# Performance work log

Measured on AMD Instinct MI355X. Metric: run time of the kernel, lower is better.

The kernel has to match this reference:

```python
import jax, jax.numpy as jnp
import numpy as np


def setup_inputs() -> dict:
    key = jax.random.key(0)
    ks = jax.random.split(key, 5)
    B, C_in, C_out, H, W, k = 16, 64, 64, 256, 256, 16
    scale = 1.0 / (C_in * C_out)
    return {
        "u": jax.random.normal(ks[0], (B, C_in, H, W), dtype=jnp.float32),
        "W_pos_re": scale * jax.random.normal(ks[1], (C_in, C_out, k, k), dtype=jnp.float32),
        "W_pos_im": scale * jax.random.normal(ks[2], (C_in, C_out, k, k), dtype=jnp.float32),
        "W_neg_re": scale * jax.random.normal(ks[3], (C_in, C_out, k, k), dtype=jnp.float32),
        "W_neg_im": scale * jax.random.normal(ks[4], (C_in, C_out, k, k), dtype=jnp.float32),
    }


def reference(u, W_pos_re, W_pos_im, W_neg_re, W_neg_im):
    B, C_in, H, W = u.shape
    C_out = W_pos_re.shape[1]
    k = W_pos_re.shape[2]
    W_half = W // 2 + 1
    k_h = min(k, H // 2)
    k_w = min(k, W_half)

    R_pos = (W_pos_re + 1j * W_pos_im)[:, :, :k_h, :k_w]  # (C_in, C_out, k_h, k_w)
    R_neg = (W_neg_re + 1j * W_neg_im)[:, :, :k_h, :k_w]

    u_hat = jnp.fft.rfft2(u, norm="ortho")  # (B, C_in, H, W_half) complex

    # spectral multiply on retained modes only
    top = jnp.einsum("bchw,cohw->bohw", u_hat[:, :, :k_h, :k_w], R_pos)
    bot = jnp.einsum("bchw,cohw->bohw", u_hat[:, :, H - k_h:, :k_w], R_neg)

    v_hat = jnp.zeros((B, C_out, H, W_half), dtype=u_hat.dtype)
    v_hat = v_hat.at[:, :, :k_h, :k_w].set(top)
    v_hat = v_hat.at[:, :, H - k_h:, :k_w].set(bot)

    return jnp.fft.irfft2(v_hat, s=(H, W), norm="ortho")  # (B, C_out, H, W) real
```

## Files before the change

### kernel.cpp

```cpp
#include <hip/hip_runtime.h>


#define B_    16
#define H_    256
#define W_    256

#define OFF_CT 0
#define OFF_ST 256
#define OFF_RP 512
#define RP_SZ  (4096*512*2)
#define OFF_U  (OFF_RP + RP_SZ)
#define U_SZ   (512*1024*2)
#define OFF_V  (OFF_U + U_SZ)

typedef const __attribute__((address_space(1))) void g_void;
typedef __attribute__((address_space(3))) void l_void;

__device__ __forceinline__ void load_lds16(const float* g, float* l) {
    __builtin_amdgcn_global_load_lds((g_void*)g, (l_void*)l, 16, 0, 0);
}

__global__ void k_twiddle(float* __restrict__ ws) {
    int t = threadIdx.x;
    double a = 2.0 * 3.14159265358979323846 * (double)t / 256.0;
    ws[OFF_CT + t] = (float)cos(a);
    ws[OFF_ST + t] = (float)sin(a);
}

__global__ __launch_bounds__(256) void k_repack(const float* __restrict__ wpr,
                                                const float* __restrict__ wpi,
                                                const float* __restrict__ wnr,
                                                const float* __restrict__ wni,
                                                float* __restrict__ ws) {
    int co = blockIdx.x, t = threadIdx.x;
    int wm = t & 15;
    float norm = (wm == 0 ? 1.f : 2.f) * (1.f / 65536.f);
    size_t src = (size_t)co * 256 + t;
    float2* rp = (float2*)(ws + OFF_RP) + (size_t)co * 512;
    rp[t]       = make_float2(wpr[src] * norm, wpi[src] * norm);
    rp[t + 256] = make_float2(wnr[src] * norm, wni[src] * norm);
}

__global__ __launch_bounds__(256) void k_fwd(const float* __restrict__ u,
                                             const float* __restrict__ ws,
                                             float* __restrict__ U) {
    __shared__ __align__(16) float ut[32][256];
    __shared__ __align__(16) float Pl[32][36];
    __shared__ float ct[256], st[256];
    int t = threadIdx.x, bc = blockIdx.x;
    ct[t] = ws[OFF_CT + t];
    st[t] = ws[OFF_ST + t];
    const float* ub = u + (size_t)bc * 65536;
    int lane = t & 63, w = t >> 6;

    #pragma unroll
    for (int k = 0; k < 8; ++k) {
        int row = w * 8 + k;
        load_lds16(ub + row * 256 + lane * 4, &ut[row][0]);
    }
    __syncthreads();

    int yl = t & 31, h = t >> 5;
    int wm0 = 2 * h, wm1 = wm0 + 1;
    int j0 = 2 * yl;
    float r0r = ct[wm0], r0i = -st[wm0];
    float r1r = ct[wm1], r1i = -st[wm1];
    float t0r0 = ct[(wm0 * j0) & 255], t0i0 = -st[(wm0 * j0) & 255];
    float t1r0 = ct[(wm1 * j0) & 255], t1i0 = -st[(wm1 * j0) & 255];
    float bs  = (h & 1) ? -1.f : 1.f;
    float dsg = (h & 1) ? 1.f : -1.f;

    int wm = t & 15, m1 = t >> 4;
    float q1r = ct[m1], q1i = -st[m1];
    int m2i = (16 - m1) & 255;
    float q2r = ct[m2i], q2i = st[m2i];
    float w1r = 1.f, w1i = 0.f, w2r = 1.f, w2i = 0.f;
    float U1r = 0.f, U1i = 0.f, U2r = 0.f, U2i = 0.f;

    for (int ch = 0; ch < 8; ++ch) {
        asm volatile("s_waitcnt vmcnt(0)" ::: "memory");
        __syncthreads();

        float t0r = t0r0, t0i = t0i0, t1r = t1r0, t1i = t1i0;
        float p0r = 0.f, p0i = 0.f, p1r = 0.f, p1i = 0.f;
        const float* row = &ut[yl][0];
        #pragma unroll 8
        for (int s = 0; s < 64; ++s) {
            int j = j0 + s;
            float u0 = row[j], u1 = row[j + 64], u2 = row[j + 128];
            float u3 = row[(j + 192) & 255];
            float a = u0 + u2, b = u1 + u3, c = u0 - u2, d = u1 - u3;
            float g0 = fmaf(bs, b, a);
            float g1r = c, g1i = dsg * d;
            p0r = fmaf(g0, t0r, p0r);
            p0i = fmaf(g0, t0i, p0i);
            p1r = fmaf(g1r, t1r, fmaf(-g1i, t1i, p1r));
            p1i = fmaf(g1r, t1i, fmaf( g1i, t1r, p1i));
            float n0r = t0r * r0r - t0i * r0i, n0i = t0r * r0i + t0i * r0r;
            float n1r = t1r * r1r - t1i * r1i, n1i = t1r * r1i + t1i * r1r;
            t0r = n0r; t0i = n0i; t1r = n1r; t1i = n1i;
        }
        *(float4*)&Pl[yl][4 * h] = make_float4(p0r, p0i, p1r, p1i);
        __syncthreads();

        if (ch < 7) {
            const float* ub2 = ub + (ch + 1) * 8192;
            #pragma unroll
            for (int k = 0; k < 8; ++k) {
                int rw = w * 8 + k;
                load_lds16(ub2 + rw * 256 + lane * 4, &ut[rw][0]);
            }
        }

        #pragma unroll 4
        for (int yy = 0; yy < 32; ++yy) {
            float2 g = *(float2*)&Pl[yy][2 * wm];
            U1r = fmaf(g.x, w1r, fmaf(-g.y, w1i, U1r));
            U1i = fmaf(g.x, w1i, fmaf( g.y, w1r, U1i));
            U2r = fmaf(g.x, w2r, fmaf(-g.y, w2i, U2r));
            U2i = fmaf(g.x, w2i, fmaf( g.y, w2r, U2i));
            float n1r = w1r * q1r - w1i * q1i, n1i = w1r * q1i + w1i * q1r;
            float n2r = w2r * q2r - w2i * q2i, n2i = w2r * q2i + w2i * q2r;
            w1r = n1r; w1i = n1i; w2r = n2r; w2i = n2i;
        }
    }

    float2* Ug = (float2*)U;
    Ug[(size_t)(m1 * 16 + wm) * 1024 + bc]        = make_float2(U1r, U1i);
    Ug[(size_t)((m1 + 16) * 16 + wm) * 1024 + bc] = make_float2(U2r, U2i);
}

__global__ __launch_bounds__(256) void k_cgemm(float* __restrict__ ws) {
    __shared__ float2 Ul[1024];
    int mw = blockIdx.x, t = threadIdx.x;
    const float2* Ug = (const float2*)(ws + OFF_U) + (size_t)mw * 1024;
    #pragma unroll
    for (int k = 0; k < 4; ++k) Ul[t + 256 * k] = Ug[t + 256 * k];
    __syncthreads();
    int o = t & 63, bq = t >> 6;
    const float2* rp = (const float2*)(ws + OFF_RP);
    float ar[4] = {0.f, 0.f, 0.f, 0.f}, ai[4] = {0.f, 0.f, 0.f, 0.f};
    #pragma unroll 4
    for (int c = 0; c < 64; ++c) {
        float2 R = rp[(size_t)(c * 64 + o) * 512 + mw];
        #pragma unroll
        for (int j = 0; j < 4; ++j) {
            float2 Uv = Ul[(bq * 4 + j) * 64 + c];
            ar[j] = fmaf(Uv.x, R.x, fmaf(-Uv.y, R.y, ar[j]));
            ai[j] = fmaf(Uv.x, R.y, fmaf( Uv.y, R.x, ai[j]));
        }
    }
    float2* Vg = (float2*)(ws + OFF_V);
    #pragma unroll
    for (int j = 0; j < 4; ++j)
        Vg[(size_t)((bq * 4 + j) * 64 + o) * 512 + mw] = make_float2(ar[j], ai[j]);
}

__global__ __launch_bounds__(256) void k_inv(const float* __restrict__ ws,
                                             float* __restrict__ out) {
    __shared__ float Vl[16][68];
    __shared__ float Tl[4][16][36];
    __shared__ float ct[256], st[256];
    int t = threadIdx.x;
    int bo = blockIdx.x >> 2, q = blockIdx.x & 3;
    ct[t] = ws[OFF_CT + t];
    st[t] = ws[OFF_ST + t];
    {
        const float2* Vg = (const float2*)(ws + OFF_V) + (size_t)bo * 512;
        float2 v0 = Vg[t];
        float2 v1 = Vg[t + 256];
        int m = t >> 4, wmv = t & 15;
        Vl[wmv][2 * m]        = v0.x;  Vl[wmv][2 * m + 1]        = v0.y;
        Vl[wmv][2 * (m + 16)] = v1.x;  Vl[wmv][2 * (m + 16) + 1] = v1.y;
    }
    __syncthreads();

    int wm4 = t & 15, yb = t >> 4;
    int y0 = q * 16 + yb;
    float vr[32], vi[32];
    #pragma unroll
    for (int m = 0; m < 32; ++m) { vr[m] = Vl[wm4][2 * m]; vi[m] = Vl[wm4][2 * m + 1]; }
    float cy = ct[y0], sy = st[y0];
    float T0r=0,T0i=0,T1r=0,T1i=0,T2r=0,T2i=0,T3r=0,T3i=0;
    float tr = 1.f, ti = 0.f;
    #pragma unroll
    for (int m = 0; m < 32; ++m) {
        if (m == 16) {
            int i16 = (4096 - 16 * y0) & 255;
            tr = ct[i16]; ti = st[i16];
        }
        float hr = vr[m] * tr - vi[m] * ti;
        float hi = vr[m] * ti + vi[m] * tr;
        const int md = m & 3;
        T0r += hr; T0i += hi;
        if (md == 0)      { T1r += hr; T1i += hi; T2r += hr; T2i += hi; T3r += hr; T3i += hi; }
        else if (md == 1) { T1r -= hi; T1i += hr; T2r -= hr; T2i -= hi; T3r += hi; T3i -= hr; }
        else if (md == 2) { T1r -= hr; T1i -= hi; T2r += hr; T2i += hi; T3r -= hr; T3i -= hi; }
        else              { T1r += hi; T1i -= hr; T2r -= hr; T2i -= hi; T3r -= hi; T3i += hr; }
        float nr = tr * cy - ti * sy, ni = tr * sy + ti * cy;
        tr = nr; ti = ni;
    }
    Tl[0][yb][wm4] = T0r; Tl[0][yb][16 + wm4] = T0i;
    Tl[1][yb][wm4] = T1r; Tl[1][yb][16 + wm4] = T1i;
    Tl[2][yb][wm4] = T2r; Tl[2][yb][16 + wm4] = T2i;
    Tl[3][yb][wm4] = T3r; Tl[3][yb][16 + wm4] = T3i;
    __syncthreads();

    int l = t & 63, wv = t >> 6;
    float c0[16], s0[16];
    #pragma unroll
    for (int wm = 0; wm < 16; ++wm) {
        int idx = (wm * l) & 255;
        c0[wm] = ct[idx]; s0[wm] = st[idx];
    }
    float* ob = out + (size_t)bo * 65536;
    for (int yi = 0; yi < 16; ++yi) {
        int y = wv * 64 + q * 16 + yi;
        float TR[16], TI[16];
        const float4* rowv = (const float4*)&Tl[wv][yi][0];
        #pragma unroll
        for (int qq = 0; qq < 4; ++qq) {
            float4 a = rowv[qq];
            TR[4*qq]=a.x; TR[4*qq+1]=a.y; TR[4*qq+2]=a.z; TR[4*qq+3]=a.w;
            float4 b = rowv[qq + 4];
            TI[4*qq]=b.x; TI[4*qq+1]=b.y; TI[4*qq+2]=b.z; TI[4*qq+3]=b.w;
        }
        #pragma unroll
        for (int k = 0; k < 4; ++k) {
            float a = 0.f;
            #pragma unroll
            for (int wm = 0; wm < 16; ++wm) {
                int p = (k * wm) & 3;
                if (p == 0)      a +=  TR[wm] * c0[wm] - TI[wm] * s0[wm];
                else if (p == 1) a += -TR[wm] * s0[wm] - TI[wm] * c0[wm];
                else if (p == 2) a += -TR[wm] * c0[wm] + TI[wm] * s0[wm];
                else             a +=  TR[wm] * s0[wm] + TI[wm] * c0[wm];
            }
            ob[(size_t)y * 256 + 64 * k + l] = a;
        }
    }
}

extern "C" void kernel_launch(void* const* d_in, const int* in_sizes, int n_in,
                              void* d_out, int out_size, void* d_ws, size_t ws_size,
                              hipStream_t stream) {
    const float* u   = (const float*)d_in[0];
    const float* wpr = (const float*)d_in[1];
    const float* wpi = (const float*)d_in[2];
    const float* wnr = (const float*)d_in[3];
    const float* wni = (const float*)d_in[4];
    float* out = (float*)d_out;
    float* ws  = (float*)d_ws;

    hipLaunchKernelGGL(k_twiddle, dim3(1),    dim3(256), 0, stream, ws);
    hipLaunchKernelGGL(k_repack,  dim3(4096), dim3(256), 0, stream, wpr, wpi, wnr, wni, ws);
    hipLaunchKernelGGL(k_fwd,     dim3(1024), dim3(256), 0, stream, u, ws, ws + OFF_U);
    hipLaunchKernelGGL(k_cgemm,   dim3(512),  dim3(256), 0, stream, ws);
    hipLaunchKernelGGL(k_inv,     dim3(4096), dim3(256), 0, stream, ws, out);
}
```

Measured before the change: 254.7 us.

## Double-buffer k_fwd input rows and remap row DFT with DPP lane reductions

The forward transform kernel now keeps two LDS buffers for input row chunks and prefetches chunk ch+2 while chunk ch is computed. Each lane now loads 8 contiguous columns once, evaluates all 16 retained width modes in registers, and sums partial results across 8 lanes with DPP shuffles. This replaces the old strided per-mode LDS reads and full-block barriers. In exchange it uses more registers (launch_bounds 2), doubles the LDS input buffer, and relies on manual vmcnt/lgkmcnt waits for correctness.

```diff
diff --git a/kernel.cpp b/kernel.cpp
--- a/kernel.cpp
+++ b/kernel.cpp
@@ -18,6 +18,12 @@
 
 __device__ __forceinline__ void load_lds16(const float* g, float* l) {
     __builtin_amdgcn_global_load_lds((g_void*)g, (l_void*)l, 16, 0, 0);
+}
+
+template<int CTRL>
+__device__ __forceinline__ float dppf(float x) {
+    return __int_as_float(__builtin_amdgcn_update_dpp(
+        0, __float_as_int(x), CTRL, 0xF, 0xF, true));
 }
 
 __global__ void k_twiddle(float* __restrict__ ws) {
@@ -41,10 +47,10 @@
     rp[t + 256] = make_float2(wnr[src] * norm, wni[src] * norm);
 }
 
-__global__ __launch_bounds__(256) void k_fwd(const float* __restrict__ u,
-                                             const float* __restrict__ ws,
-                                             float* __restrict__ U) {
-    __shared__ __align__(16) float ut[32][256];
+__global__ __launch_bounds__(256, 2) void k_fwd(const float* __restrict__ u,
+                                                const float* __restrict__ ws,
+                                                float* __restrict__ U) {
+    __shared__ __align__(16) float ut[2][32][256];
     __shared__ __align__(16) float Pl[32][36];
     __shared__ float ct[256], st[256];
     int t = threadIdx.x, bc = blockIdx.x;
@@ -52,25 +58,28 @@
     st[t] = ws[OFF_ST + t];
     const float* ub = u + (size_t)bc * 65536;
     int lane = t & 63, w = t >> 6;
-
-    #pragma unroll
-    for (int k = 0; k < 8; ++k) {
-        int row = w * 8 + k;
-        load_lds16(ub + row * 256 + lane * 4, &ut[row][0]);
-    }
-    __syncthreads();
-
-    int yl = t & 31, h = t >> 5;
-    int wm0 = 2 * h, wm1 = wm0 + 1;
-    int j0 = 2 * yl;
-    float r0r = ct[wm0], r0i = -st[wm0];
-    float r1r = ct[wm1], r1i = -st[wm1];
-    float t0r0 = ct[(wm0 * j0) & 255], t0i0 = -st[(wm0 * j0) & 255];
-    float t1r0 = ct[(wm1 * j0) & 255], t1i0 = -st[(wm1 * j0) & 255];
-    float bs  = (h & 1) ? -1.f : 1.f;
-    float dsg = (h & 1) ? 1.f : -1.f;
-
-    int wm = t & 15, m1 = t >> 4;
+    int seg = lane & 7, ylw = lane >> 3;
+    int rowc = w * 8 + ylw;
+
+    #pragma unroll
+    for (int k = 0; k < 8; ++k)
+        load_lds16(ub + (w * 8 + k) * 256 + lane * 4, &ut[0][w * 8 + k][0]);
+    #pragma unroll
+    for (int k = 0; k < 8; ++k)
+        load_lds16(ub + 8192 + (w * 8 + k) * 256 + lane * 4, &ut[1][w * 8 + k][0]);
+
+    asm volatile("s_waitcnt lgkmcnt(0)" ::: "memory");
+    __builtin_amdgcn_s_barrier();
+
+    float rr[16], ri[16], t0r[16], t0i[16];
+    #pragma unroll
+    for (int wm = 0; wm < 16; ++wm) {
+        rr[wm] = ct[wm]; ri[wm] = -st[wm];
+        int a0 = (wm * 8 * seg) & 255;
+        t0r[wm] = ct[a0]; t0i[wm] = -st[a0];
+    }
+
+    int wm2 = t & 15, m1 = t >> 4;
     float q1r = ct[m1], q1i = -st[m1];
     int m2i = (16 - m1) & 255;
     float q2r = ct[m2i], q2i = st[m2i];
@@ -78,43 +87,91 @@
     float U1r = 0.f, U1i = 0.f, U2r = 0.f, U2i = 0.f;
 
     for (int ch = 0; ch < 8; ++ch) {
-        asm volatile("s_waitcnt vmcnt(0)" ::: "memory");
-        __syncthreads();
-
-        float t0r = t0r0, t0i = t0i0, t1r = t1r0, t1i = t1i0;
-        float p0r = 0.f, p0i = 0.f, p1r = 0.f, p1i = 0.f;
-        const float* row = &ut[yl][0];
-        #pragma unroll 8
-        for (int s = 0; s < 64; ++s) {
-            int j = j0 + s;
-            float u0 = row[j], u1 = row[j + 64], u2 = row[j + 128];
-            float u3 = row[(j + 192) & 255];
-            float a = u0 + u2, b = u1 + u3, c = u0 - u2, d = u1 - u3;
-            float g0 = fmaf(bs, b, a);
-            float g1r = c, g1i = dsg * d;
-            p0r = fmaf(g0, t0r, p0r);
-            p0i = fmaf(g0, t0i, p0i);
-            p1r = fmaf(g1r, t1r, fmaf(-g1i, t1i, p1r));
-            p1i = fmaf(g1r, t1i, fmaf( g1i, t1r, p1i));
-            float n0r = t0r * r0r - t0i * r0i, n0i = t0r * r0i + t0i * r0r;
-            float n1r = t1r * r1r - t1i * r1i, n1i = t1r * r1i + t1i * r1r;
-            t0r = n0r; t0i = n0i; t1r = n1r; t1i = n1i;
-        }
-        *(float4*)&Pl[yl][4 * h] = make_float4(p0r, p0i, p1r, p1i);
-        __syncthreads();
-
-        if (ch < 7) {
-            const float* ub2 = ub + (ch + 1) * 8192;
+        const int buf = ch & 1;
+        if (ch < 7) asm volatile("s_waitcnt vmcnt(8)" ::: "memory");
+        else        asm volatile("s_waitcnt vmcnt(0)" ::: "memory");
+
+        float AP[8], AM[8], C[8], D[8];
+        {
+            const float* rp = &ut[buf][rowc][8 * seg];
+            float4 x0  = *(const float4*)(rp);
+            float4 x0b = *(const float4*)(rp + 4);
+            float4 x1  = *(const float4*)(rp + 64);
+            float4 x1b = *(const float4*)(rp + 68);
+            float4 x2  = *(const float4*)(rp + 128);
+            float4 x2b = *(const float4*)(rp + 132);
+            float4 x3  = *(const float4*)(rp + 192);
+            float4 x3b = *(const float4*)(rp + 196);
+            #define QT_(i, u0, u1, u2, u3) { float a_=(u0)+(u2), b_=(u1)+(u3); \
+                C[i]=(u0)-(u2); D[i]=(u1)-(u3); AP[i]=a_+b_; AM[i]=a_-b_; }
+            QT_(0, x0.x,  x1.x,  x2.x,  x3.x)
+            QT_(1, x0.y,  x1.y,  x2.y,  x3.y)
+            QT_(2, x0.z,  x1.z,  x2.z,  x3.z)
+            QT_(3, x0.w,  x1.w,  x2.w,  x3.w)
+            QT_(4, x0b.x, x1b.x, x2b.x, x3b.x)
+            QT_(5, x0b.y, x1b.y, x2b.y, x3b.y)
+            QT_(6, x0b.z, x1b.z, x2b.z, x3b.z)
+            QT_(7, x0b.w, x1b.w, x2b.w, x3b.w)
+            #undef QT_
+        }
+
+        if (ch < 6) {
+            const float* ub2 = ub + (ch + 2) * 8192;
             #pragma unroll
-            for (int k = 0; k < 8; ++k) {
-                int rw = w * 8 + k;
-                load_lds16(ub2 + rw * 256 + lane * 4, &ut[rw][0]);
+            for (int k = 0; k < 8; ++k)
+                load_lds16(ub2 + (w * 8 + k) * 256 + lane * 4, &ut[buf][w * 8 + k][0]);
+        }
+
+        float P[32];
+        #pragma unroll
+        for (int wm = 0; wm < 16; ++wm) {
+            float twr = t0r[wm], twi = t0i[wm];
+            float Pr = 0.f, Pi = 0.f;
+            #pragma unroll
+            for (int s = 0; s < 8; ++s) {
+                if ((wm & 1) == 0) {
+                    float g = (wm & 2) ? AM[s] : AP[s];
+                    Pr = fmaf(g, twr, Pr);
+                    Pi = fmaf(g, twi, Pi);
+                } else if ((wm & 2) == 0) {
+                    Pr = fmaf(C[s], twr, fmaf( D[s], twi, Pr));
+                    Pi = fmaf(C[s], twi, fmaf(-D[s], twr, Pi));
+                } else {
+                    Pr = fmaf(C[s], twr, fmaf(-D[s], twi, Pr));
+                    Pi = fmaf(C[s], twi, fmaf( D[s], twr, Pi));
+                }
+                float nr = twr * rr[wm] - twi * ri[wm];
+                float ni = twr * ri[wm] + twi * rr[wm];
+                twr = nr; twi = ni;
             }
-        }
+            P[2 * wm] = Pr; P[2 * wm + 1] = Pi;
+        }
+
+        #pragma unroll
+        for (int i = 0; i < 32; ++i) {
+            float v = P[i];
+            v += dppf<0xB1>(v);
+            v += dppf<0x4E>(v);
+            v += dppf<0x141>(v);
+            P[i] = v;
+        }
+        if (seg == 0) {
+            float4* pr = (float4*)&Pl[rowc][0];
+            pr[0] = make_float4(P[0],  P[1],  P[2],  P[3]);
+            pr[1] = make_float4(P[4],  P[5],  P[6],  P[7]);
+            pr[2] = make_float4(P[8],  P[9],  P[10], P[11]);
+            pr[3] = make_float4(P[12], P[13], P[14], P[15]);
+            pr[4] = make_float4(P[16], P[17], P[18], P[19]);
+            pr[5] = make_float4(P[20], P[21], P[22], P[23]);
+            pr[6] = make_float4(P[24], P[25], P[26], P[27]);
+            pr[7] = make_float4(P[28], P[29], P[30], P[31]);
+        }
+        asm volatile("s_waitcnt lgkmcnt(0)" ::: "memory");
+        __builtin_amdgcn_s_barrier();
 
         #pragma unroll 4
         for (int yy = 0; yy < 32; ++yy) {
-            float2 g = *(float2*)&Pl[yy][2 * wm];
+            float2 g = *(float2*)&Pl[yy][2 * wm2];
             U1r = fmaf(g.x, w1r, fmaf(-g.y, w1i, U1r));
             U1i = fmaf(g.x, w1i, fmaf( g.y, w1r, U1i));
             U2r = fmaf(g.x, w2r, fmaf(-g.y, w2i, U2r));
@@ -123,11 +180,12 @@
             float n2r = w2r * q2r - w2i * q2i, n2i = w2r * q2i + w2i * q2r;
             w1r = n1r; w1i = n1i; w2r = n2r; w2i = n2i;
         }
+        __builtin_amdgcn_s_barrier();
     }
 
     float2* Ug = (float2*)U;
-    Ug[(size_t)(m1 * 16 + wm) * 1024 + bc]        = make_float2(U1r, U1i);
-    Ug[(size_t)((m1 + 16) * 16 + wm) * 1024 + bc] = make_float2(U2r, U2i);
+    Ug[(size_t)(m1 * 16 + wm2) * 1024 + bc]        = make_float2(U1r, U1i);
+    Ug[(size_t)((m1 + 16) * 16 + wm2) * 1024 + bc] = make_float2(U2r, U2i);
 }
 
 __global__ __launch_bounds__(256) void k_cgemm(float* __restrict__ ws) {
```

Result: slower. 741.9 us (+191.3%).

## Double-buffer forward DFT input tile and vectorize row reads in k_fwd

Applied to the files above, without the earlier changes.

Adds a second LDS buffer for the input chunk in the forward-transform kernel. The chunk two steps ahead is prefetched with global_load_lds while the current one is processed, and partial waits (vmcnt(8)) replace the full drain plus barrier. Each thread is remapped so a wave only reads rows it loaded itself. Row reads become padded float4 accesses, and the kernel gets launch_bounds(256,2). The larger LDS footprint and the occupancy hint trade against the latency hiding.

```diff
diff --git a/kernel.cpp b/kernel.cpp
--- a/kernel.cpp
+++ b/kernel.cpp
@@ -12,6 +12,8 @@
 #define OFF_U  (OFF_RP + RP_SZ)
 #define U_SZ   (512*1024*2)
 #define OFF_V  (OFF_U + U_SZ)
+
+#define UTP   260
 
 typedef const __attribute__((address_space(1))) void g_void;
 typedef __attribute__((address_space(3))) void l_void;
@@ -41,10 +43,10 @@
     rp[t + 256] = make_float2(wnr[src] * norm, wni[src] * norm);
 }
 
-__global__ __launch_bounds__(256) void k_fwd(const float* __restrict__ u,
-                                             const float* __restrict__ ws,
-                                             float* __restrict__ U) {
-    __shared__ __align__(16) float ut[32][256];
+__global__ __launch_bounds__(256, 2) void k_fwd(const float* __restrict__ u,
+                                                const float* __restrict__ ws,
+                                                float* __restrict__ U) {
+    __shared__ __align__(16) float ut[2][32][UTP];
     __shared__ __align__(16) float Pl[32][36];
     __shared__ float ct[256], st[256];
     int t = threadIdx.x, bc = blockIdx.x;
@@ -52,25 +54,26 @@
     st[t] = ws[OFF_ST + t];
     const float* ub = u + (size_t)bc * 65536;
     int lane = t & 63, w = t >> 6;
-
-    #pragma unroll
-    for (int k = 0; k < 8; ++k) {
-        int row = w * 8 + k;
-        load_lds16(ub + row * 256 + lane * 4, &ut[row][0]);
-    }
-    __syncthreads();
-
-    int yl = t & 31, h = t >> 5;
+    int h = lane & 7, r8 = lane >> 3;
+    int rowc = w * 8 + r8;
+
+    #pragma unroll
+    for (int k = 0; k < 8; ++k)
+        load_lds16(ub + (w * 8 + k) * 256 + lane * 4, &ut[0][w * 8 + k][0]);
+    #pragma unroll
+    for (int k = 0; k < 8; ++k)
+        load_lds16(ub + 8192 + (w * 8 + k) * 256 + lane * 4, &ut[1][w * 8 + k][0]);
+
+    asm volatile("s_waitcnt lgkmcnt(0)" ::: "memory");
+    __builtin_amdgcn_s_barrier();
+
     int wm0 = 2 * h, wm1 = wm0 + 1;
-    int j0 = 2 * yl;
     float r0r = ct[wm0], r0i = -st[wm0];
     float r1r = ct[wm1], r1i = -st[wm1];
-    float t0r0 = ct[(wm0 * j0) & 255], t0i0 = -st[(wm0 * j0) & 255];
-    float t1r0 = ct[(wm1 * j0) & 255], t1i0 = -st[(wm1 * j0) & 255];
     float bs  = (h & 1) ? -1.f : 1.f;
     float dsg = (h & 1) ? 1.f : -1.f;
 
-    int wm = t & 15, m1 = t >> 4;
+    int wm2 = t & 15, m1 = t >> 4;
     float q1r = ct[m1], q1i = -st[m1];
     int m2i = (16 - m1) & 255;
     float q2r = ct[m2i], q2i = st[m2i];
@@ -78,43 +81,55 @@
     float U1r = 0.f, U1i = 0.f, U2r = 0.f, U2i = 0.f;
 
     for (int ch = 0; ch < 8; ++ch) {
-        asm volatile("s_waitcnt vmcnt(0)" ::: "memory");
-        __syncthreads();
-
-        float t0r = t0r0, t0i = t0i0, t1r = t1r0, t1i = t1i0;
+        const int buf = ch & 1;
+        if (ch < 7) asm volatile("s_waitcnt vmcnt(8)" ::: "memory");
+        else        asm volatile("s_waitcnt vmcnt(0)" ::: "memory");
+
         float p0r = 0.f, p0i = 0.f, p1r = 0.f, p1i = 0.f;
-        const float* row = &ut[yl][0];
-        #pragma unroll 8
-        for (int s = 0; s < 64; ++s) {
-            int j = j0 + s;
-            float u0 = row[j], u1 = row[j + 64], u2 = row[j + 128];
-            float u3 = row[(j + 192) & 255];
-            float a = u0 + u2, b = u1 + u3, c = u0 - u2, d = u1 - u3;
-            float g0 = fmaf(bs, b, a);
-            float g1r = c, g1i = dsg * d;
-            p0r = fmaf(g0, t0r, p0r);
-            p0i = fmaf(g0, t0i, p0i);
-            p1r = fmaf(g1r, t1r, fmaf(-g1i, t1i, p1r));
-            p1i = fmaf(g1r, t1i, fmaf( g1i, t1r, p1i));
-            float n0r = t0r * r0r - t0i * r0i, n0i = t0r * r0i + t0i * r0r;
-            float n1r = t1r * r1r - t1i * r1i, n1i = t1r * r1i + t1i * r1r;
-            t0r = n0r; t0i = n0i; t1r = n1r; t1i = n1i;
-        }
-        *(float4*)&Pl[yl][4 * h] = make_float4(p0r, p0i, p1r, p1i);
-        __syncthreads();
-
-        if (ch < 7) {
-            const float* ub2 = ub + (ch + 1) * 8192;
+        float t0r = 1.f, t0i = 0.f, t1r = 1.f, t1i = 0.f;
+        const float* rowp = &ut[buf][rowc][0];
+        #pragma unroll 4
+        for (int bat = 0; bat < 16; ++bat) {
+            const float* rp = rowp + 4 * bat;
+            float4 q0 = *(const float4*)(rp);
+            float4 q1 = *(const float4*)(rp + 64);
+            float4 q2 = *(const float4*)(rp + 128);
+            float4 q3 = *(const float4*)(rp + 192);
+            #define PROC_(u0, u1, u2, u3) {                                   \
+                float a_ = (u0) + (u2), b_ = (u1) + (u3);                     \
+                float c_ = (u0) - (u2), d_ = (u1) - (u3);                     \
+                float g0 = fmaf(bs, b_, a_);                                  \
+                float g1r = c_, g1i = dsg * d_;                               \
+                p0r = fmaf(g0, t0r, p0r);                                     \
+                p0i = fmaf(g0, t0i, p0i);                                     \
+                p1r = fmaf(g1r, t1r, fmaf(-g1i, t1i, p1r));                   \
+                p1i = fmaf(g1r, t1i, fmaf( g1i, t1r, p1i));                   \
+                float n0r = t0r * r0r - t0i * r0i;                            \
+                float n0i = t0r * r0i + t0i * r0r;                            \
+                float n1r = t1r * r1r - t1i * r1i;                            \
+                float n1i = t1r * r1i + t1i * r1r;                            \
+                t0r = n0r; t0i = n0i; t1r = n1r; t1i = n1i; }
+            PROC_(q0.x, q1.x, q2.x, q3.x)
+            PROC_(q0.y, q1.y, q2.y, q3.y)
+            PROC_(q0.z, q1.z, q2.z, q3.z)
+            PROC_(q0.w, q1.w, q2.w, q3.w)
+            #undef PROC_
+        }
+
+        if (ch < 6) {
+            const float* ub2 = ub + (ch + 2) * 8192;
             #pragma unroll
-            for (int k = 0; k < 8; ++k) {
-                int rw = w * 8 + k;
-                load_lds16(ub2 + rw * 256 + lane * 4, &ut[rw][0]);
-            }
-        }
+            for (int k = 0; k < 8; ++k)
+                load_lds16(ub2 + (w * 8 + k) * 256 + lane * 4, &ut[buf][w * 8 + k][0]);
+        }
+
+        *(float4*)&Pl[rowc][4 * h] = make_float4(p0r, p0i, p1r, p1i);
+        asm volatile("s_waitcnt lgkmcnt(0)" ::: "memory");
+        __builtin_amdgcn_s_barrier();
 
         #pragma unroll 4
         for (int yy = 0; yy < 32; ++yy) {
-            float2 g = *(float2*)&Pl[yy][2 * wm];
+            float2 g = *(float2*)&Pl[yy][2 * wm2];
             U1r = fmaf(g.x, w1r, fmaf(-g.y, w1i, U1r));
             U1i = fmaf(g.x, w1i, fmaf( g.y, w1r, U1i));
             U2r = fmaf(g.x, w2r, fmaf(-g.y, w2i, U2r));
@@ -123,11 +138,12 @@
             float n2r = w2r * q2r - w2i * q2i, n2i = w2r * q2i + w2i * q2r;
             w1r = n1r; w1i = n1i; w2r = n2r; w2i = n2i;
         }
+        __builtin_amdgcn_s_barrier();
     }
 
     float2* Ug = (float2*)U;
-    Ug[(size_t)(m1 * 16 + wm) * 1024 + bc]        = make_float2(U1r, U1i);
-    Ug[(size_t)((m1 + 16) * 16 + wm) * 1024 + bc] = make_float2(U2r, U2i);
+    Ug[(size_t)(m1 * 16 + wm2) * 1024 + bc]        = make_float2(U1r, U1i);
+    Ug[(size_t)((m1 + 16) * 16 + wm2) * 1024 + bc] = make_float2(U2r, U2i);
 }
 
 __global__ __launch_bounds__(256) void k_cgemm(float* __restrict__ ws) {
```

After: 254.9 us. No clear change (+0.1%).
